# Kernel tuning notes

Measured on AMD Instinct MI355X. Metric: run time of the kernel, lower is better.

## Reference

```python
import jax, jax.numpy as jnp
import numpy as np

POOLED_H = 7
POOLED_W = 7
SPATIAL_SCALE = 0.0625  # 1/16
SAMPLING_RATIO = 2      # fixed sample grid (Detectron default), jit-friendly


def setup_inputs() -> dict:
    key = jax.random.key(0)
    k1, k2, k3, k4 = jax.random.split(key, 4)
    N, C, H, W = 2, 256, 200, 200
    features = jax.random.normal(k1, (N, C, H, W), dtype=jnp.float32)
    num_rois = 1000
    img = H / SPATIAL_SCALE  # image-space extent = 3200
    bidx = jax.random.randint(k2, (num_rois,), 0, N).astype(jnp.float32)
    xy1 = jax.random.uniform(k3, (num_rois, 2), dtype=jnp.float32) * (img * 0.8)
    wh = jax.random.uniform(k4, (num_rois, 2), dtype=jnp.float32) * (img * 0.2) + 16.0
    xy2 = jnp.minimum(xy1 + wh, img - 1.0)
    # rois: [num_rois, 5] = (batch_idx, x1, y1, x2, y2)
    rois = jnp.concatenate([bidx[:, None], xy1[:, 0:1], xy1[:, 1:2], xy2[:, 0:1], xy2[:, 1:2]], axis=1)
    return {"features": features, "rois": rois}


def _bilinear(img, ys, xs):
    # img: [C,H,W]; ys, xs: [P] sample coords in feature-map space
    C, H, W = img.shape
    valid = (ys > -1.0) & (ys < H) & (xs > -1.0) & (xs < W)
    y = jnp.clip(ys, 0.0)
    x = jnp.clip(xs, 0.0)
    y0 = jnp.minimum(jnp.floor(y).astype(jnp.int32), H - 1)
    x0 = jnp.minimum(jnp.floor(x).astype(jnp.int32), W - 1)
    y1 = jnp.minimum(y0 + 1, H - 1)
    x1 = jnp.minimum(x0 + 1, W - 1)
    # CUDA kernel snaps y to y_low when y_low >= H-1 (same for x)
    y = jnp.where(y0 >= H - 1, y0.astype(y.dtype), y)
    x = jnp.where(x0 >= W - 1, x0.astype(x.dtype), x)
    ly = y - y0
    lx = x - x0
    hy = 1.0 - ly
    hx = 1.0 - lx
    # gathers: [C, P]
    v = (hy * hx) * img[:, y0, x0] + (hy * lx) * img[:, y0, x1] \
        + (ly * hx) * img[:, y1, x0] + (ly * lx) * img[:, y1, x1]
    return jnp.where(valid, v, 0.0)


def _roi_align_one(features, roi):
    b = roi[0].astype(jnp.int32)
    img = jnp.take(features, b, axis=0)  # [C,H,W]
    x1 = roi[1] * SPATIAL_SCALE
    y1 = roi[2] * SPATIAL_SCALE
    x2 = roi[3] * SPATIAL_SCALE
    y2 = roi[4] * SPATIAL_SCALE
    roi_w = jnp.maximum(x2 - x1, 1.0)
    roi_h = jnp.maximum(y2 - y1, 1.0)
    bin_h = roi_h / POOLED_H
    bin_w = roi_w / POOLED_W
    r = SAMPLING_RATIO
    # sample coords: [PH, r] and [PW, r]
    yy = y1 + jnp.arange(POOLED_H, dtype=jnp.float32)[:, None] * bin_h \
         + (jnp.arange(r, dtype=jnp.float32)[None, :] + 0.5) * bin_h / r
    xx = x1 + jnp.arange(POOLED_W, dtype=jnp.float32)[:, None] * bin_w \
         + (jnp.arange(r, dtype=jnp.float32)[None, :] + 0.5) * bin_w / r
    Yg, Xg = jnp.meshgrid(yy.ravel(), xx.ravel(), indexing="ij")  # [PH*r, PW*r]
    vals = _bilinear(img, Yg.ravel(), Xg.ravel())  # [C, PH*r*PW*r]
    C = img.shape[0]
    vals = vals.reshape(C, POOLED_H, r, POOLED_W, r).mean(axis=(2, 4))
    return vals  # [C, PH, PW]


def reference(features, rois):
    # -> [num_rois, C, pooled_h, pooled_w]
    return jax.vmap(_roi_align_one, in_axes=(None, 0))(features, rois)
```

## Files before the change

kernel.cpp:

```cpp
#include <hip/hip_runtime.h>


#define POOLED_H 7
#define POOLED_W 7
#define SPATIAL_SCALE 0.0625f
#define FEAT_N 2
#define FEAT_C 256
#define FEAT_H 200
#define FEAT_W 200
#define FEAT_S (FEAT_H * FEAT_W)
#define IMG_USH ((size_t)FEAT_S * FEAT_C)

#define ST 64
#define ST4 (ST / 4)
#define CT 128
#define SROW 66

__device__ __forceinline__ unsigned short f2bf(float f) {
    unsigned int u = __float_as_uint(f);
    u += 0x7fffu + ((u >> 16) & 1u);
    return (unsigned short)(u >> 16);
}

__device__ __forceinline__ float bflo(unsigned int u) { return __uint_as_float(u << 16); }
__device__ __forceinline__ float bfhi(unsigned int u) { return __uint_as_float(u & 0xffff0000u); }

__global__ __launch_bounds__(256) void nchw_to_nhwc_bf16(
        const float* __restrict__ in, unsigned short* __restrict__ outp) {
    __shared__ unsigned short lds[CT * SROW];
    const int s0 = blockIdx.x * ST;
    const int c0 = blockIdx.y * CT;
    const int b = blockIdx.z;
    const int tid = threadIdx.x;

    const float* ibase = in + ((size_t)(b * FEAT_C + c0)) * FEAT_S + s0;
    float4 v[8];
#pragma unroll
    for (int k = 0; k < 8; ++k) {
        int f = tid + 256 * k;
        int c = f >> 4;
        int j = f & 15;
        v[k] = *(const float4*)(ibase + (size_t)c * FEAT_S + 4 * j);
    }
#pragma unroll
    for (int k = 0; k < 8; ++k) {
        int f = tid + 256 * k;
        int c = f >> 4;
        int j = f & 15;
        unsigned int p0 = (unsigned)f2bf(v[k].x) | ((unsigned)f2bf(v[k].y) << 16);
        unsigned int p1 = (unsigned)f2bf(v[k].z) | ((unsigned)f2bf(v[k].w) << 16);
        unsigned short* lp = &lds[c * SROW + 4 * j];
        *(unsigned int*)(lp) = p0;
        *(unsigned int*)(lp + 2) = p1;
    }
    __syncthreads();

    unsigned short* obase = outp + ((size_t)b * FEAT_S + s0) * FEAT_C + c0;
#pragma unroll
    for (int k = 0; k < 2; ++k) {
        int f = tid + 256 * k;
        int sp = f >> 4;
        int m = f & 15;
        const unsigned short* lp = &lds[(8 * m) * SROW + 2 * sp];
        unsigned int d0 = *(const unsigned int*)(lp);
        unsigned int d1 = *(const unsigned int*)(lp + SROW);
        unsigned int d2 = *(const unsigned int*)(lp + 2 * SROW);
        unsigned int d3 = *(const unsigned int*)(lp + 3 * SROW);
        unsigned int d4 = *(const unsigned int*)(lp + 4 * SROW);
        unsigned int d5 = *(const unsigned int*)(lp + 5 * SROW);
        unsigned int d6 = *(const unsigned int*)(lp + 6 * SROW);
        unsigned int d7 = *(const unsigned int*)(lp + 7 * SROW);
        unsigned int w0 = (d0 & 0xffffu) | (d1 << 16);
        unsigned int w1 = (d2 & 0xffffu) | (d3 << 16);
        unsigned int w2 = (d4 & 0xffffu) | (d5 << 16);
        unsigned int w3 = (d6 & 0xffffu) | (d7 << 16);
        *(uint4*)(obase + (size_t)(2 * sp) * FEAT_C + 8 * m) = make_uint4(w0, w1, w2, w3);
        unsigned int u0 = (d0 >> 16) | (d1 & 0xffff0000u);
        unsigned int u1 = (d2 >> 16) | (d3 & 0xffff0000u);
        unsigned int u2 = (d4 >> 16) | (d5 & 0xffff0000u);
        unsigned int u3 = (d6 >> 16) | (d7 & 0xffff0000u);
        *(uint4*)(obase + (size_t)(2 * sp + 1) * FEAT_C + 8 * m) = make_uint4(u0, u1, u2, u3);
    }
}

__global__ __launch_bounds__(256) void roialign_main(
        const unsigned short* __restrict__ feat,
        const float* __restrict__ rois,
        float* __restrict__ out,
        int num_rois) {
    __shared__ float outbuf[64 * 49];
    __shared__ unsigned int s_rowlo[14], s_rowhi[14];
    __shared__ unsigned int s_collo[14], s_colhi[14];
    __shared__ float s_ywl[14], s_ywh[14], s_xwl[14], s_xwh[14];

    const int bid = blockIdx.x;
    const int roi = bid >> 2;
    const int qc = (bid & 3) * 64;

    const float* r = rois + roi * 5;
    const int b = (int)r[0];
    const float x1 = r[1] * SPATIAL_SCALE;
    const float y1 = r[2] * SPATIAL_SCALE;
    const float x2 = r[3] * SPATIAL_SCALE;
    const float y2 = r[4] * SPATIAL_SCALE;
    const float bin_w = fmaxf(x2 - x1, 1.0f) * (1.0f / POOLED_W);
    const float bin_h = fmaxf(y2 - y1, 1.0f) * (1.0f / POOLED_H);

    const int tid = threadIdx.x;
    if (tid < 14) {
        int p = tid >> 1, i = tid & 1;
        float yy = y1 + (float)p * bin_h + ((float)i + 0.5f) * bin_h * 0.5f;
        bool v = (yy > -1.0f) && (yy < (float)FEAT_H);
        float y = fmaxf(yy, 0.0f);
        int lo = min((int)floorf(y), FEAT_H - 1);
        int hi = min(lo + 1, FEAT_H - 1);
        if (lo >= FEAT_H - 1) y = (float)lo;
        float l = y - (float)lo;
        s_rowlo[tid] = (unsigned)(lo * (FEAT_W * FEAT_C));
        s_rowhi[tid] = (unsigned)(hi * (FEAT_W * FEAT_C));
        s_ywl[tid] = v ? l : 0.0f;
        s_ywh[tid] = v ? (1.0f - l) : 0.0f;
    } else if (tid >= 64 && tid < 78) {
        int tt = tid - 64;
        int p = tt >> 1, i = tt & 1;
        float xx = x1 + (float)p * bin_w + ((float)i + 0.5f) * bin_w * 0.5f;
        bool v = (xx > -1.0f) && (xx < (float)FEAT_W);
        float x = fmaxf(xx, 0.0f);
        int lo = min((int)floorf(x), FEAT_W - 1);
        int hi = min(lo + 1, FEAT_W - 1);
        if (lo >= FEAT_W - 1) x = (float)lo;
        float l = x - (float)lo;
        s_collo[tt] = (unsigned)(lo * FEAT_C);
        s_colhi[tt] = (unsigned)(hi * FEAT_C);
        s_xwl[tt] = v ? l : 0.0f;
        s_xwh[tt] = v ? (1.0f - l) : 0.0f;
    }
    __syncthreads();

    const int g = tid & 7;
    const int slot = tid >> 3;
    const unsigned int cbase = (unsigned)((size_t)b * IMG_USH) + (unsigned)(qc + 8 * g);

#pragma unroll
    for (int k = 0; k < 2; ++k) {
        const int s = slot + 32 * k;
        if (s < 49) {
            const int ph = (s * 37) >> 8;
            const int pw = s - ph * 7;
            float a0 = 0.f, a1 = 0.f, a2 = 0.f, a3 = 0.f;
            float a4 = 0.f, a5 = 0.f, a6 = 0.f, a7 = 0.f;
#pragma unroll
            for (int iy = 0; iy < 2; ++iy) {
                const int ky = ph * 2 + iy;
                const unsigned int rl = cbase + s_rowlo[ky];
                const unsigned int rh = cbase + s_rowhi[ky];
                const float wyl = s_ywl[ky];
                const float wyh = s_ywh[ky];
#pragma unroll
                for (int ix = 0; ix < 2; ++ix) {
                    const int kx = pw * 2 + ix;
                    const unsigned int cl = s_collo[kx];
                    const unsigned int ch = s_colhi[kx];
                    const float w00 = wyh * s_xwh[kx];
                    const float w01 = wyh * s_xwl[kx];
                    const float w10 = wyl * s_xwh[kx];
                    const float w11 = wyl * s_xwl[kx];
                    uint4 t00 = *(const uint4*)(feat + (size_t)(rl + cl));
                    uint4 t01 = *(const uint4*)(feat + (size_t)(rl + ch));
                    uint4 t10 = *(const uint4*)(feat + (size_t)(rh + cl));
                    uint4 t11 = *(const uint4*)(feat + (size_t)(rh + ch));
                    a0 += w00 * bflo(t00.x) + w01 * bflo(t01.x) + w10 * bflo(t10.x) + w11 * bflo(t11.x);
                    a1 += w00 * bfhi(t00.x) + w01 * bfhi(t01.x) + w10 * bfhi(t10.x) + w11 * bfhi(t11.x);
                    a2 += w00 * bflo(t00.y) + w01 * bflo(t01.y) + w10 * bflo(t10.y) + w11 * bflo(t11.y);
                    a3 += w00 * bfhi(t00.y) + w01 * bfhi(t01.y) + w10 * bfhi(t10.y) + w11 * bfhi(t11.y);
                    a4 += w00 * bflo(t00.z) + w01 * bflo(t01.z) + w10 * bflo(t10.z) + w11 * bflo(t11.z);
                    a5 += w00 * bfhi(t00.z) + w01 * bfhi(t01.z) + w10 * bfhi(t10.z) + w11 * bfhi(t11.z);
                    a6 += w00 * bflo(t00.w) + w01 * bflo(t01.w) + w10 * bflo(t10.w) + w11 * bflo(t11.w);
                    a7 += w00 * bfhi(t00.w) + w01 * bfhi(t01.w) + w10 * bfhi(t10.w) + w11 * bfhi(t11.w);
                }
            }
            const int cb = 8 * g;
            outbuf[(cb + 0) * 49 + s] = a0 * 0.25f;
            outbuf[(cb + 1) * 49 + s] = a1 * 0.25f;
            outbuf[(cb + 2) * 49 + s] = a2 * 0.25f;
            outbuf[(cb + 3) * 49 + s] = a3 * 0.25f;
            outbuf[(cb + 4) * 49 + s] = a4 * 0.25f;
            outbuf[(cb + 5) * 49 + s] = a5 * 0.25f;
            outbuf[(cb + 6) * 49 + s] = a6 * 0.25f;
            outbuf[(cb + 7) * 49 + s] = a7 * 0.25f;
        }
    }
    __syncthreads();

    const float4* src = (const float4*)outbuf;
    float4* dst = (float4*)(out + (size_t)(roi * FEAT_C + qc) * 49);
    for (int i = tid; i < 784; i += 256) dst[i] = src[i];
}

__device__ __forceinline__ float bilinear_tap(const float* __restrict__ plane,
                                              float y, float x) {
    const int H = FEAT_H, W = FEAT_W;
    if (!(y > -1.0f && y < (float)H && x > -1.0f && x < (float)W)) return 0.0f;
    y = fmaxf(y, 0.0f);
    x = fmaxf(x, 0.0f);
    int y0 = min((int)floorf(y), H - 1);
    int x0 = min((int)floorf(x), W - 1);
    int y1 = min(y0 + 1, H - 1);
    int x1 = min(x0 + 1, W - 1);
    if (y0 >= H - 1) y = (float)y0;
    if (x0 >= W - 1) x = (float)x0;
    float ly = y - (float)y0, lx = x - (float)x0;
    float hy = 1.0f - ly, hx = 1.0f - lx;
    return hy * (hx * plane[y0 * W + x0] + lx * plane[y0 * W + x1]) +
           ly * (hx * plane[y1 * W + x0] + lx * plane[y1 * W + x1]);
}

__global__ __launch_bounds__(256) void roialign_direct(
    const float* __restrict__ features, const float* __restrict__ rois,
    float* __restrict__ out, int num_rois) {
    int i = blockIdx.x * blockDim.x + threadIdx.x;
    int total = num_rois * FEAT_C * 49;
    if (i >= total) return;
    int s = i % 49;
    int t = i / 49;
    int c = t % FEAT_C;
    int roi = t / FEAT_C;
    int ph = s / POOLED_W, pw = s % POOLED_W;
    const float* r = rois + roi * 5;
    int b = (int)r[0];
    float x1 = r[1] * SPATIAL_SCALE, y1 = r[2] * SPATIAL_SCALE;
    float x2 = r[3] * SPATIAL_SCALE, y2 = r[4] * SPATIAL_SCALE;
    float bin_w = fmaxf(x2 - x1, 1.0f) * (1.0f / POOLED_W);
    float bin_h = fmaxf(y2 - y1, 1.0f) * (1.0f / POOLED_H);
    const float* plane = features + ((size_t)(b * FEAT_C + c)) * FEAT_S;
    float acc = 0.0f;
#pragma unroll
    for (int iy = 0; iy < 2; ++iy) {
        float yy = y1 + (float)ph * bin_h + ((float)iy + 0.5f) * bin_h * 0.5f;
#pragma unroll
        for (int ix = 0; ix < 2; ++ix) {
            float xx = x1 + (float)pw * bin_w + ((float)ix + 0.5f) * bin_w * 0.5f;
            acc += bilinear_tap(plane, yy, xx);
        }
    }
    out[i] = acc * 0.25f;
}

extern "C" void kernel_launch(void* const* d_in, const int* in_sizes, int n_in,
                              void* d_out, int out_size, void* d_ws, size_t ws_size,
                              hipStream_t stream) {
    const float* features = (const float*)d_in[0];
    const float* rois = (const float*)d_in[1];
    float* out = (float*)d_out;
    int num_rois = in_sizes[1] / 5;
    size_t need = (size_t)FEAT_N * IMG_USH * sizeof(unsigned short);
    if (ws_size >= need) {
        unsigned short* nhwc = (unsigned short*)d_ws;
        nchw_to_nhwc_bf16<<<dim3(FEAT_S / ST, FEAT_C / CT, FEAT_N), 256, 0, stream>>>(
            features, nhwc);
        roialign_main<<<num_rois * 4, 256, 0, stream>>>(nhwc, rois, out, num_rois);
    } else {
        int total = num_rois * FEAT_C * 49;
        roialign_direct<<<(total + 255) / 256, 256, 0, stream>>>(features, rois, out,
                                                                 num_rois);
    }
}
```

Before: 161.8 us.

## Sort ROIs by spatial bin and remap workgroups to XCDs for cache locality

Adds a single-block counting-sort kernel that groups ROIs by batch index and an 8x8 spatial bin of their centres, then has the main kernel read ROIs through that permutation. Workgroup IDs are also remapped so consecutive sorted ROIs land on the same XCD (assuming round-robin dispatch across 8 XCDs), so spatially nearby ROIs share that XCD's L2. The goal is to cut redundant feature-map fetches from HBM/MALL. The cost is an extra serial kernel launch and an indirect ROI lookup.

Result: no change. 160.2 us (-1.0%).

```diff
diff --git a/kernel.cpp b/kernel.cpp
--- a/kernel.cpp
+++ b/kernel.cpp
@@ -16,6 +16,8 @@
 #define CT 128
 #define SROW 66
 
+#define NBINS 128
+
 __device__ __forceinline__ unsigned short f2bf(float f) {
     unsigned int u = __float_as_uint(f);
     u += 0x7fffu + ((u >> 16) & 1u);
@@ -24,6 +26,36 @@
 
 __device__ __forceinline__ float bflo(unsigned int u) { return __uint_as_float(u << 16); }
 __device__ __forceinline__ float bfhi(unsigned int u) { return __uint_as_float(u & 0xffff0000u); }
+
+__device__ __forceinline__ int roi_bin(const float* __restrict__ r) {
+    int b = (int)r[0];
+    b = min(max(b, 0), FEAT_N - 1);
+    float cy = (r[2] + r[4]) * 0.5f * SPATIAL_SCALE;
+    float cx = (r[1] + r[3]) * 0.5f * SPATIAL_SCALE;
+    int yc = min(max((int)(cy * (8.0f / (float)FEAT_H)), 0), 7);
+    int xc = min(max((int)(cx * (8.0f / (float)FEAT_W)), 0), 7);
+    return (b << 6) | (yc << 3) | xc;
+}
+
+__global__ __launch_bounds__(1024) void roi_sort(
+        const float* __restrict__ rois, int num_rois, int* __restrict__ perm) {
+    __shared__ int hist[NBINS];
+    const int tid = threadIdx.x;
+    if (tid < NBINS) hist[tid] = 0;
+    __syncthreads();
+    for (int i = tid; i < num_rois; i += 1024)
+        atomicAdd(&hist[roi_bin(rois + i * 5)], 1);
+    __syncthreads();
+    if (tid == 0) {
+        int acc = 0;
+        for (int i = 0; i < NBINS; ++i) { int c = hist[i]; hist[i] = acc; acc += c; }
+    }
+    __syncthreads();
+    for (int i = tid; i < num_rois; i += 1024) {
+        int pos = atomicAdd(&hist[roi_bin(rois + i * 5)], 1);
+        perm[pos] = i;
+    }
+}
 
 __global__ __launch_bounds__(256) void nchw_to_nhwc_bf16(
         const float* __restrict__ in, unsigned short* __restrict__ outp) {
@@ -86,6 +118,7 @@
 __global__ __launch_bounds__(256) void roialign_main(
         const unsigned short* __restrict__ feat,
         const float* __restrict__ rois,
+        const int* __restrict__ perm,
         float* __restrict__ out,
         int num_rois) {
     __shared__ float outbuf[64 * 49];
@@ -93,8 +126,13 @@
     __shared__ unsigned int s_collo[14], s_colhi[14];
     __shared__ float s_ywl[14], s_ywh[14], s_xwl[14], s_xwh[14];
 
-    const int bid = blockIdx.x;
-    const int roi = bid >> 2;
+    int bid = blockIdx.x;
+    const int nwg = gridDim.x;
+    if ((nwg & 7) == 0) {
+        const int cpx = nwg >> 3;
+        bid = (bid & 7) * cpx + (bid >> 3);
+    }
+    const int roi = perm[bid >> 2];
     const int qc = (bid & 3) * 64;
 
     const float* r = rois + roi * 5;
@@ -253,12 +291,15 @@
     const float* rois = (const float*)d_in[1];
     float* out = (float*)d_out;
     int num_rois = in_sizes[1] / 5;
-    size_t need = (size_t)FEAT_N * IMG_USH * sizeof(unsigned short);
+    size_t nhwc_bytes = (size_t)FEAT_N * IMG_USH * sizeof(unsigned short);
+    size_t need = nhwc_bytes + (size_t)num_rois * sizeof(int);
     if (ws_size >= need) {
         unsigned short* nhwc = (unsigned short*)d_ws;
+        int* perm = (int*)((char*)d_ws + nhwc_bytes);
+        roi_sort<<<1, 1024, 0, stream>>>(rois, num_rois, perm);
         nchw_to_nhwc_bf16<<<dim3(FEAT_S / ST, FEAT_C / CT, FEAT_N), 256, 0, stream>>>(
             features, nhwc);
-        roialign_main<<<num_rois * 4, 256, 0, stream>>>(nhwc, rois, out, num_rois);
+        roialign_main<<<num_rois * 4, 256, 0, stream>>>(nhwc, rois, perm, out, num_rois);
     } else {
         int total = num_rois * FEAT_C * 49;
         roialign_direct<<<(total + 255) / 256, 256, 0, stream>>>(features, rois, out,
```
